# Kernel optimization log

Hardware: AMD Instinct MI355X
Metric: run time of the kernel (lower is better)

The kernel has to match this reference:

```python
import jax, jax.numpy as jnp
import numpy as np

N_NODES = 100000
N_EDGES = 1600000
D_IN, D_H1, D_H2 = 128, 64, 16


def setup_inputs() -> dict:
    key = jax.random.key(0)
    ks = jax.random.split(key, 12)
    def glorot(k, shape):
        fan_in, fan_out = shape
        lim = np.sqrt(6.0 / (fan_in + fan_out)).astype(np.float32)
        return jax.random.uniform(k, shape, jnp.float32, -lim, lim)
    x = jax.random.normal(ks[0], (N_NODES, D_IN), jnp.float32)
    edge_index = jax.random.randint(ks[1], (2, N_EDGES), 0, N_NODES, jnp.int64)
    return {
        "x": x,
        "edge_index": edge_index,
        # SAGEConv1: lin_l (neighbor agg, has bias), lin_r (root, no bias) -- stored (in,out)
        "w1_l": glorot(ks[2], (D_IN, D_H1)),
        "w1_r": glorot(ks[3], (D_IN, D_H1)),
        "b1": jnp.zeros((D_H1,), jnp.float32),
        # SAGEConv2
        "w2_l": glorot(ks[4], (D_H1, D_H2)),
        "w2_r": glorot(ks[5], (D_H1, D_H2)),
        "b2": jnp.zeros((D_H2,), jnp.float32),
        # MLP head
        "fc1_w": glorot(ks[6], (D_H2, 8)),
        "fc1_b": jnp.zeros((8,), jnp.float32),
        "fc2_w": glorot(ks[7], (8, 1)),
        "fc2_b": jnp.zeros((1,), jnp.float32),
    }


def _sage_conv(h, src, dst, n_nodes, w_l, w_r, b):
    # mean aggregation of source-node features into destination nodes
    msgs = h[src]                                                  # [E, d]
    agg = jax.ops.segment_sum(msgs, dst, num_segments=n_nodes)     # [N, d]
    deg = jax.ops.segment_sum(jnp.ones((src.shape[0],), h.dtype), dst,
                              num_segments=n_nodes)                # [N]
    mean = agg / jnp.maximum(deg, 1.0)[:, None]
    return mean @ w_l + h @ w_r + b


def reference(x, edge_index, w1_l, w1_r, b1, w2_l, w2_r, b2,
              fc1_w, fc1_b, fc2_w, fc2_b):
    src, dst = edge_index[0], edge_index[1]
    n = x.shape[0]
    h = _sage_conv(x, src, dst, n, w1_l, w1_r, b1)   # [N, 64]
    h = _sage_conv(h, src, dst, n, w2_l, w2_r, b2)   # [N, 16]
    # embedding_mlp on edge endpoint embeddings
    e = h[src] * h[dst]                              # [E, 16]
    out = (e @ fc1_w + fc1_b) @ fc2_w + fc2_b        # [E, 1]
    return jax.nn.sigmoid(out)
```

## Files before the change

kernel.cpp:

```cpp
#include <hip/hip_runtime.h>
#include <hip/hip_fp16.h>
#include <math.h>

#define NN 100000
#define NE 1600000

#define BSH  9
#define BKN  512
#define NB   196
#define ABLK 128
#define EPB  ((NE + ABLK - 1) / ABLK)
#define GEMMB ((NN + 63) / 64)
#define GBLK ((GEMMB + 1) / 2)
#define LDST 136

typedef __attribute__((ext_vector_type(8))) short bf16x8;
typedef __attribute__((ext_vector_type(4))) float f32x4;

__device__ __forceinline__ unsigned short f2bf(float f) {
    unsigned u = __builtin_bit_cast(unsigned, f);
    u += 0x7fffu + ((u >> 16) & 1u);
    return (unsigned short)(u >> 16);
}
__device__ __forceinline__ float bf2f(unsigned short h) {
    unsigned u = ((unsigned)h) << 16;
    return __builtin_bit_cast(float, u);
}
__device__ __forceinline__ float2 unpackh2(unsigned w) {
    const __half2 h = __builtin_bit_cast(__half2, w);
    return __half22float2(h);
}

__global__ __launch_bounds__(256) void fused0(const int* __restrict__ dst,
    const float* __restrict__ w1l, const float* __restrict__ w1r,
    const float* __restrict__ w2l, const float* __restrict__ w2r,
    const float* __restrict__ b1, const float* __restrict__ fc1w,
    const float* __restrict__ fc1b, const float* __restrict__ fc2w,
    const float* __restrict__ fc2b, int* __restrict__ mat,
    unsigned short* __restrict__ ATh, unsigned short* __restrict__ ATl,
    float* __restrict__ cbuf)
{
    __shared__ int h[NB];
    __shared__ float sl[64], sr[64];
    const int t = threadIdx.x;
    if (blockIdx.x < ABLK) {
        for (int i = t; i < NB; i += 256) h[i] = 0;
        __syncthreads();
        const int a = blockIdx.x;
        const int beg = a * EPB;
        const int end = (beg + EPB < NE) ? beg + EPB : NE;
        int e = beg + t;
        for (; e + 3 * 256 < end; e += 4 * 256) {
            const int d0 = dst[e], d1 = dst[e + 256], d2 = dst[e + 512], d3 = dst[e + 768];
            atomicAdd(&h[d0 >> BSH], 1);
            atomicAdd(&h[d1 >> BSH], 1);
            atomicAdd(&h[d2 >> BSH], 1);
            atomicAdd(&h[d3 >> BSH], 1);
        }
        for (; e < end; e += 256)
            atomicAdd(&h[dst[e] >> BSH], 1);
        __syncthreads();
        for (int i = t; i < NB; i += 256) mat[(size_t)i * ABLK + a] = h[i];
        return;
    }
    if (blockIdx.x < ABLK + 128) {
        const int k = blockIdx.x - ABLK;
        const int j = t;
        if (j < 64) { sl[j] = w1l[k * 64 + j]; sr[j] = w1r[k * 64 + j]; }
        __syncthreads();
        if (j < 64) {
            const int sel = j >> 4, jj = j & 15;
            const float* row = (sel < 2) ? sl : sr;
            const float* w2  = (sel & 1) ? w2r : w2l;
            float acc = 0.f;
#pragma unroll
            for (int m = 0; m < 64; ++m) acc = fmaf(row[m], w2[m * 16 + jj], acc);
            const unsigned short hh = f2bf(acc);
            ATh[j * 128 + k] = hh;
            ATl[j * 128 + k] = f2bf(acc - bf2f(hh));
        }
        return;
    }
    const int j = t;
    if (j < 16) {
        float a = 0.f;
        for (int m = 0; m < 64; ++m) a = fmaf(b1[m], w2l[m * 16 + j], a);
        cbuf[j] = a;
    } else if (j < 32) {
        const int jj = j - 16;
        float a = 0.f;
        for (int m = 0; m < 64; ++m) a = fmaf(b1[m], w2r[m * 16 + jj], a);
        cbuf[j] = a;
    } else if (j < 48) {
        const int k = j - 32;
        float a = 0.f;
        for (int m = 0; m < 8; ++m) a = fmaf(fc1w[k * 8 + m], fc2w[m], a);
        cbuf[j] = a;
    } else if (j == 48) {
        float a = fc2b[0];
        for (int m = 0; m < 8; ++m) a = fmaf(fc1b[m], fc2w[m], a);
        cbuf[48] = a;
    }
}

__global__ __launch_bounds__(256) void scan_all(int* __restrict__ mat,
    int* __restrict__ bbase)
{
    __shared__ int s[256];
    const int t = threadIdx.x;
    int run = 0;
    if (t < NB) {
        int* col = mat + (size_t)t * ABLK;
        for (int a = 0; a < ABLK; ++a) { const int v = col[a]; col[a] = run; run += v; }
    }
    s[t] = (t < NB) ? run : 0;
    __syncthreads();
    for (int off = 1; off < 256; off <<= 1) {
        const int u = (t >= off) ? s[t - off] : 0;
        __syncthreads();
        s[t] += u;
        __syncthreads();
    }
    if (t < NB) bbase[t] = s[t] - run;
    if (t == NB - 1) bbase[NB] = s[t];
}

__global__ __launch_bounds__(512) void fused1(const int* __restrict__ src,
    const int* __restrict__ dst, const int* __restrict__ mat,
    const int* __restrict__ bbase, unsigned* __restrict__ part,
    const float* __restrict__ x, const unsigned short* __restrict__ ATh,
    const unsigned short* __restrict__ ATl, signed char* __restrict__ p8,
    float* __restrict__ pscale, __half* __restrict__ qh)
{
    __shared__ unsigned short sAh[64 * LDST];
    __shared__ unsigned short sAl[64 * LDST];
    __shared__ int cur[NB];
    const int tid = threadIdx.x;

    if (blockIdx.x < ABLK) {
        const int a = blockIdx.x;
        for (int i = tid; i < NB; i += 512)
            cur[i] = mat[(size_t)i * ABLK + a] + bbase[i];
        __syncthreads();
        const int beg = a * EPB;
        const int end = (beg + EPB < NE) ? beg + EPB : NE;
        int e = beg + tid;
        for (; e + 3 * 512 < end; e += 4 * 512) {
            const int s0 = src[e],          d0 = dst[e];
            const int s1 = src[e + 512],    d1 = dst[e + 512];
            const int s2 = src[e + 1024],   d2 = dst[e + 1024];
            const int s3 = src[e + 1536],   d3 = dst[e + 1536];
            const int p0 = atomicAdd(&cur[d0 >> BSH], 1);
            const int p1 = atomicAdd(&cur[d1 >> BSH], 1);
            const int p2 = atomicAdd(&cur[d2 >> BSH], 1);
            const int p3 = atomicAdd(&cur[d3 >> BSH], 1);
            part[p0] = ((unsigned)s0 << BSH) | (unsigned)(d0 & (BKN - 1));
            part[p1] = ((unsigned)s1 << BSH) | (unsigned)(d1 & (BKN - 1));
            part[p2] = ((unsigned)s2 << BSH) | (unsigned)(d2 & (BKN - 1));
            part[p3] = ((unsigned)s3 << BSH) | (unsigned)(d3 & (BKN - 1));
        }
        for (; e < end; e += 512) {
            const int s = src[e], d = dst[e];
            const int pos = atomicAdd(&cur[d >> BSH], 1);
            part[pos] = ((unsigned)s << BSH) | (unsigned)(d & (BKN - 1));
        }
        return;
    }

    for (int i = tid; i < 1024; i += 512) {
        const int row = i >> 4, ch = i & 15;
        const uint4 vh = *(const uint4*)(ATh + row * 128 + ch * 8);
        const uint4 vl = *(const uint4*)(ATl + row * 128 + ch * 8);
        *(uint4*)(sAh + row * LDST + ch * 8) = vh;
        *(uint4*)(sAl + row * LDST + ch * 8) = vl;
    }
    __syncthreads();

    const int wave8 = tid >> 6;
    const int tile = (blockIdx.x - ABLK) * 2 + (wave8 >> 2);
    const int wave = wave8 & 3;
    const int lane = tid & 63;
    const int lr = lane & 15;
    const int lg = lane >> 4;

    bf16x8 bh[4][4], bl[4][4];
#pragma unroll
    for (int ct = 0; ct < 4; ++ct) {
        const int col = ct * 16 + lr;
#pragma unroll
        for (int ks = 0; ks < 4; ++ks) {
            const int k0 = ks * 32 + lg * 8;
            bh[ct][ks] = *(const bf16x8*)(sAh + col * LDST + k0);
            bl[ct][ks] = *(const bf16x8*)(sAl + col * LDST + k0);
        }
    }

    if (tile >= GEMMB) return;
    const int tilebase = tile * 64;
    const int xrowidx = tilebase + wave * 16 + lr;
    const float* xrow = x + (size_t)(xrowidx < NN ? xrowidx : NN - 1) * 128;

    f32x4 acc[4] = {f32x4{0,0,0,0}, f32x4{0,0,0,0}, f32x4{0,0,0,0}, f32x4{0,0,0,0}};
#pragma unroll
    for (int ks = 0; ks < 4; ++ks) {
        const int k0 = ks * 32 + lg * 8;
        const float4 v0 = *(const float4*)(xrow + k0);
        const float4 v1 = *(const float4*)(xrow + k0 + 4);
        const float vv[8] = {v0.x, v0.y, v0.z, v0.w, v1.x, v1.y, v1.z, v1.w};
        bf16x8 xh, xl;
#pragma unroll
        for (int j = 0; j < 8; ++j) {
            const unsigned short h = f2bf(vv[j]);
            xh[j] = (short)h;
            xl[j] = (short)f2bf(vv[j] - bf2f(h));
        }
#pragma unroll
        for (int ct = 0; ct < 4; ++ct) {
            acc[ct] = __builtin_amdgcn_mfma_f32_16x16x32_bf16(xh, bh[ct][ks], acc[ct], 0, 0, 0);
            acc[ct] = __builtin_amdgcn_mfma_f32_16x16x32_bf16(xh, bl[ct][ks], acc[ct], 0, 0, 0);
            acc[ct] = __builtin_amdgcn_mfma_f32_16x16x32_bf16(xl, bh[ct][ks], acc[ct], 0, 0, 0);
        }
    }

#pragma unroll
    for (int rg = 0; rg < 4; ++rg) {
        float m = fmaxf(fabsf(acc[0][rg]), fabsf(acc[1][rg]));
#pragma unroll
        for (int d = 1; d < 16; d <<= 1) m = fmaxf(m, __shfl_xor(m, d, 64));
        m = fmaxf(m, 1e-20f);
        const float scl = m * (1.0f / 127.0f);
        const float inv = 127.0f / m;
        const int nrow = tilebase + wave * 16 + lg * 4 + rg;
        if (nrow < NN) {
            const int q0 = __float2int_rn(acc[0][rg] * inv);
            const int q1 = __float2int_rn(acc[1][rg] * inv);
            p8[(size_t)nrow * 32 + lr]      = (signed char)q0;
            p8[(size_t)nrow * 32 + 16 + lr] = (signed char)q1;
            if (lr == 0) pscale[nrow] = scl;
            qh[(size_t)nrow * 32 + lr]      = __float2half(acc[2][rg]);
            qh[(size_t)nrow * 32 + 16 + lr] = __float2half(acc[3][rg]);
        }
    }
}

__global__ __launch_bounds__(512) void partB_build(const unsigned* __restrict__ part,
    const int* __restrict__ bbase, int* __restrict__ rowptr, int* __restrict__ cols)
{
    __shared__ int h[BKN];
    __shared__ int cur[BKN];
    __shared__ int wsum[8];
    const int b = blockIdx.x;
    const int t = threadIdx.x;
    const int beg = bbase[b], end = bbase[b + 1];
    h[t] = 0;
    __syncthreads();
    {
        int e = beg + t;
        for (; e + 3 * 512 < end; e += 4 * 512) {
            const unsigned w0 = part[e], w1 = part[e + 512];
            const unsigned w2 = part[e + 1024], w3 = part[e + 1536];
            atomicAdd(&h[w0 & (BKN - 1u)], 1);
            atomicAdd(&h[w1 & (BKN - 1u)], 1);
            atomicAdd(&h[w2 & (BKN - 1u)], 1);
            atomicAdd(&h[w3 & (BKN - 1u)], 1);
        }
        for (; e < end; e += 512)
            atomicAdd(&h[part[e] & (BKN - 1u)], 1);
    }
    __syncthreads();
    const int v = h[t];
    int inc = v;
#pragma unroll
    for (int d = 1; d < 64; d <<= 1) {
        const int u = __shfl_up(inc, d, 64);
        if ((t & 63) >= d) inc += u;
    }
    if ((t & 63) == 63) wsum[t >> 6] = inc;
    __syncthreads();
    int woff = 0;
    for (int w = 0; w < (t >> 6); ++w) woff += wsum[w];
    const int excl = inc + woff - v;
    cur[t] = excl;
    const int node = b * BKN + t;
    if (node < NN) rowptr[node] = beg + excl;
    if (b == NB - 1 && t == 0) rowptr[NN] = NE;
    __syncthreads();
    {
        int e = beg + t;
        for (; e + 3 * 512 < end; e += 4 * 512) {
            const unsigned w0 = part[e], w1 = part[e + 512];
            const unsigned w2 = part[e + 1024], w3 = part[e + 1536];
            const int p0 = atomicAdd(&cur[w0 & (BKN - 1u)], 1);
            const int p1 = atomicAdd(&cur[w1 & (BKN - 1u)], 1);
            const int p2 = atomicAdd(&cur[w2 & (BKN - 1u)], 1);
            const int p3 = atomicAdd(&cur[w3 & (BKN - 1u)], 1);
            cols[beg + p0] = (int)(w0 >> BSH);
            cols[beg + p1] = (int)(w1 >> BSH);
            cols[beg + p2] = (int)(w2 >> BSH);
            cols[beg + p3] = (int)(w3 >> BSH);
        }
        for (; e < end; e += 512) {
            const unsigned w = part[e];
            const int pos = atomicAdd(&cur[w & (BKN - 1u)], 1);
            cols[beg + pos] = (int)(w >> BSH);
        }
    }
}

__global__ __launch_bounds__(256) void agg1_csr(const int* __restrict__ rowptr,
    const int* __restrict__ cols, const signed char* __restrict__ p8,
    const float* __restrict__ pscale, const __half* __restrict__ qh,
    const float* __restrict__ cbuf, __half* __restrict__ g, __half* __restrict__ r)
{
    const int node = blockIdx.x * 8 + (threadIdx.x >> 5);
    if (node >= NN) return;
    const int lane = threadIdx.x & 31;
    const int es = lane >> 2;
    const int k  = lane & 3;
    const int beg = rowptr[node], end = rowptr[node + 1];
    const int deg = end - beg;
    const int grpbase = threadIdx.x & 32;
    const int myc = (lane < deg) ? cols[beg + lane] : 0;
    const uint2* p64 = (const uint2*)p8;
    float a0 = 0.f, a1 = 0.f, a2 = 0.f, a3 = 0.f;
    float a4 = 0.f, a5 = 0.f, a6 = 0.f, a7 = 0.f;
#pragma unroll 2
    for (int base = 0; base < deg; base += 8) {
        const int idx = base + es;
        const bool valid = idx < deg;
        int s;
        if (idx < 32) s = __shfl(myc, grpbase + idx, 64);
        else          s = cols[beg + (valid ? idx : deg - 1)];
        const float scl = valid ? pscale[s] : 0.f;
        const uint2 w = p64[(size_t)s * 4 + k];
        a0 = fmaf((float)(signed char)(w.x & 0xffu), scl, a0);
        a1 = fmaf((float)(signed char)((w.x >> 8) & 0xffu), scl, a1);
        a2 = fmaf((float)(signed char)((w.x >> 16) & 0xffu), scl, a2);
        a3 = fmaf((float)(signed char)(w.x >> 24), scl, a3);
        a4 = fmaf((float)(signed char)(w.y & 0xffu), scl, a4);
        a5 = fmaf((float)(signed char)((w.y >> 8) & 0xffu), scl, a5);
        a6 = fmaf((float)(signed char)((w.y >> 16) & 0xffu), scl, a6);
        a7 = fmaf((float)(signed char)(w.y >> 24), scl, a7);
    }
#pragma unroll
    for (int d = 4; d <= 16; d <<= 1) {
        a0 += __shfl_xor(a0, d, 64); a1 += __shfl_xor(a1, d, 64);
        a2 += __shfl_xor(a2, d, 64); a3 += __shfl_xor(a3, d, 64);
        a4 += __shfl_xor(a4, d, 64); a5 += __shfl_xor(a5, d, 64);
        a6 += __shfl_xor(a6, d, 64); a7 += __shfl_xor(a7, d, 64);
    }
    if (es == 0) {
        const float dg = (float)deg;
        const float inv = 1.0f / fmaxf(dg, 1.0f);
        const uint4 qw = *(const uint4*)(qh + (size_t)node * 32 + 8 * k);
        const float2 q0 = unpackh2(qw.x), q1 = unpackh2(qw.y);
        const float2 q2 = unpackh2(qw.z), q3 = unpackh2(qw.w);
        const float4 cb0 = *(const float4*)(cbuf + 8 * k);
        const float4 cb1 = *(const float4*)(cbuf + 8 * k + 4);
        const float v0 = fmaf(a0, inv, q0.x + cb0.x);
        const float v1 = fmaf(a1, inv, q0.y + cb0.y);
        const float v2 = fmaf(a2, inv, q1.x + cb0.z);
        const float v3 = fmaf(a3, inv, q1.y + cb0.w);
        const float v4 = fmaf(a4, inv, q2.x + cb1.x);
        const float v5 = fmaf(a5, inv, q2.y + cb1.y);
        const float v6 = fmaf(a6, inv, q3.x + cb1.z);
        const float v7 = fmaf(a7, inv, q3.y + cb1.w);
        uint4 ow;
        ow.x = __builtin_bit_cast(unsigned, __floats2half2_rn(v0, v1));
        ow.y = __builtin_bit_cast(unsigned, __floats2half2_rn(v2, v3));
        ow.z = __builtin_bit_cast(unsigned, __floats2half2_rn(v4, v5));
        ow.w = __builtin_bit_cast(unsigned, __floats2half2_rn(v6, v7));
        if (k < 2) *(uint4*)(g + (size_t)node * 16 + 8 * k) = ow;
        else       *(uint4*)(r + (size_t)node * 16 + 8 * (k - 2)) = ow;
    }
}

__global__ __launch_bounds__(256) void agg2_csr(const int* __restrict__ rowptr,
    const int* __restrict__ cols, const __half* __restrict__ g,
    const __half* __restrict__ r, const float* __restrict__ b2,
    __half* __restrict__ h2)
{
    const int node = blockIdx.x * 8 + (threadIdx.x >> 5);
    if (node >= NN) return;
    const int lane = threadIdx.x & 31;
    const int es = lane >> 2;
    const int k  = lane & 3;
    const int beg = rowptr[node], end = rowptr[node + 1];
    const int deg = end - beg;
    const int grpbase = threadIdx.x & 32;
    const int myc = (lane < deg) ? cols[beg + lane] : 0;
    const uint2* g64 = (const uint2*)g;
    float a0 = 0.f, a1 = 0.f, a2 = 0.f, a3 = 0.f;
#pragma unroll 2
    for (int base = 0; base < deg; base += 8) {
        const int idx = base + es;
        const bool valid = idx < deg;
        int s;
        if (idx < 32) s = __shfl(myc, grpbase + idx, 64);
        else          s = cols[beg + (valid ? idx : deg - 1)];
        const float m = valid ? 1.0f : 0.0f;
        const uint2 w = g64[(size_t)s * 4 + k];
        const float2 v0 = unpackh2(w.x);
        const float2 v1 = unpackh2(w.y);
        a0 = fmaf(v0.x, m, a0);
        a1 = fmaf(v0.y, m, a1);
        a2 = fmaf(v1.x, m, a2);
        a3 = fmaf(v1.y, m, a3);
    }
#pragma unroll
    for (int d = 4; d <= 16; d <<= 1) {
        a0 += __shfl_xor(a0, d, 64); a1 += __shfl_xor(a1, d, 64);
        a2 += __shfl_xor(a2, d, 64); a3 += __shfl_xor(a3, d, 64);
    }
    if (es == 0) {
        const float dg = (float)deg;
        const float inv = 1.0f / fmaxf(dg, 1.0f);
        const uint2 rw = ((const uint2*)r)[(size_t)node * 4 + k];
        const float2 r0 = unpackh2(rw.x), r1 = unpackh2(rw.y);
        const float4 bb = *(const float4*)(b2 + 4 * k);
        const float v0 = fmaf(a0, inv, r0.x + bb.x);
        const float v1 = fmaf(a1, inv, r0.y + bb.y);
        const float v2 = fmaf(a2, inv, r1.x + bb.z);
        const float v3 = fmaf(a3, inv, r1.y + bb.w);
        uint2 ow;
        ow.x = __builtin_bit_cast(unsigned, __floats2half2_rn(v0, v1));
        ow.y = __builtin_bit_cast(unsigned, __floats2half2_rn(v2, v3));
        ((uint2*)h2)[(size_t)node * 4 + k] = ow;
    }
}

__global__ __launch_bounds__(256) void edge_mlp(const int* __restrict__ src,
    const int* __restrict__ dst, const __half* __restrict__ h2,
    const float* __restrict__ cbuf, float* __restrict__ out)
{
    __shared__ float sv[17];
    if (threadIdx.x < 16) sv[threadIdx.x] = cbuf[32 + threadIdx.x];
    if (threadIdx.x == 16) sv[16] = cbuf[48];
    __syncthreads();
    const int ebase = blockIdx.x * 1024 + threadIdx.x;
#pragma unroll
    for (int u = 0; u < 4; ++u) {
        const int e = ebase + u * 256;
        if (e >= NE) return;
        const int s = src[e], d = dst[e];
        const uint4* hs = (const uint4*)(h2 + (size_t)s * 16);
        const uint4* hd = (const uint4*)(h2 + (size_t)d * 16);
        const uint4 a0 = hs[0], a1 = hs[1];
        const uint4 b0 = hd[0], b1 = hd[1];
        const unsigned aw[8] = {a0.x, a0.y, a0.z, a0.w, a1.x, a1.y, a1.z, a1.w};
        const unsigned bw[8] = {b0.x, b0.y, b0.z, b0.w, b1.x, b1.y, b1.z, b1.w};
        float acc = sv[16];
#pragma unroll
        for (int qq = 0; qq < 8; ++qq) {
            const float2 a = unpackh2(aw[qq]);
            const float2 b = unpackh2(bw[qq]);
            acc = fmaf(a.x * b.x, sv[qq * 2 + 0], acc);
            acc = fmaf(a.y * b.y, sv[qq * 2 + 1], acc);
        }
        out[e] = 1.0f / (1.0f + __expf(-acc));
    }
}

extern "C" void kernel_launch(void* const* d_in, const int* in_sizes, int n_in,
                              void* d_out, int out_size, void* d_ws, size_t ws_size,
                              hipStream_t stream)
{
    const float* x    = (const float*)d_in[0];
    const int*   ei   = (const int*)d_in[1];
    const float* w1l  = (const float*)d_in[2];
    const float* w1r  = (const float*)d_in[3];
    const float* b1   = (const float*)d_in[4];
    const float* w2l  = (const float*)d_in[5];
    const float* w2r  = (const float*)d_in[6];
    const float* b2   = (const float*)d_in[7];
    const float* fc1w = (const float*)d_in[8];
    const float* fc1b = (const float*)d_in[9];
    const float* fc2w = (const float*)d_in[10];
    const float* fc2b = (const float*)d_in[11];
    float* out = (float*)d_out;

    const int* src = ei;
    const int* dst = ei + NE;

    int* W = (int*)d_ws;
    size_t o = 0;
#define ALIGN16() o = (o + 15) & ~(size_t)15
    int* mat    = W + o; o += (size_t)NB * ABLK; ALIGN16();
    int* bbase  = W + o; o += NB + 1;            ALIGN16();
    int* rowptr = W + o; o += NN + 1;            ALIGN16();
    unsigned* part = (unsigned*)(W + o); o += NE; ALIGN16();
    int* cols   = W + o; o += NE;                ALIGN16();
    unsigned short* ATh = (unsigned short*)(W + o); o += 4096; ALIGN16();
    unsigned short* ATl = (unsigned short*)(W + o); o += 4096; ALIGN16();
    float* cbuf = (float*)(W + o); o += 64;      ALIGN16();
    signed char* p8 = (signed char*)(W + o); o += (size_t)NN * 8;  ALIGN16();
    float* pscale   = (float*)(W + o); o += NN;  ALIGN16();
    __half* qh  = (__half*)(W + o); o += (size_t)NN * 16; ALIGN16();
    __half* g   = (__half*)(W + o); o += (size_t)NN * 8;  ALIGN16();
    __half* r   = (__half*)(W + o); o += (size_t)NN * 8;  ALIGN16();
    __half* h2  = (__half*)(W + o); o += (size_t)NN * 8;  ALIGN16();

    fused0<<<ABLK + 129, 256, 0, stream>>>(dst, w1l, w1r, w2l, w2r, b1,
                                           fc1w, fc1b, fc2w, fc2b, mat, ATh, ATl, cbuf);
    scan_all<<<1, 256, 0, stream>>>(mat, bbase);
    fused1<<<ABLK + GBLK, 512, 0, stream>>>(src, dst, mat, bbase, part,
                                            x, ATh, ATl, p8, pscale, qh);
    partB_build<<<NB, 512, 0, stream>>>(part, bbase, rowptr, cols);
    agg1_csr<<<(NN + 7) / 8, 256, 0, stream>>>(rowptr, cols, p8, pscale, qh, cbuf, g, r);
    agg2_csr<<<(NN + 7) / 8, 256, 0, stream>>>(rowptr, cols, g, r, b2, h2);
    edge_mlp<<<(NE + 1023) / 1024, 256, 0, stream>>>(src, dst, h2, cbuf, out);
}
```

Baseline: 126.2 us.

## Fold bucket scan into partition kernel and halve destination bucket width

Removes the single-block scan_all launch. Each partition block of fused1 now recomputes its own column prefix and a block-wide scan of bucket totals, and block 0 writes bbase. The bucket size drops from 512 to 256 nodes, giving 391 buckets, so partB_build runs more, smaller blocks with half its threads idle. This trades one kernel launch plus a serial scan for redundant per-block scan work in every partition block.

After: 122.1 us. 3.2% less time.

```diff
diff --git a/kernel.cpp b/kernel.cpp
--- a/kernel.cpp
+++ b/kernel.cpp
@@ -5,9 +5,9 @@
 #define NN 100000
 #define NE 1600000
 
-#define BSH  9
-#define BKN  512
-#define NB   196
+#define BSH  8
+#define BKN  256
+#define NB   391
 #define ABLK 128
 #define EPB  ((NE + ABLK - 1) / ABLK)
 #define GEMMB ((NN + 63) / 64)
@@ -103,31 +103,9 @@
     }
 }
 
-__global__ __launch_bounds__(256) void scan_all(int* __restrict__ mat,
-    int* __restrict__ bbase)
-{
-    __shared__ int s[256];
-    const int t = threadIdx.x;
-    int run = 0;
-    if (t < NB) {
-        int* col = mat + (size_t)t * ABLK;
-        for (int a = 0; a < ABLK; ++a) { const int v = col[a]; col[a] = run; run += v; }
-    }
-    s[t] = (t < NB) ? run : 0;
-    __syncthreads();
-    for (int off = 1; off < 256; off <<= 1) {
-        const int u = (t >= off) ? s[t - off] : 0;
-        __syncthreads();
-        s[t] += u;
-        __syncthreads();
-    }
-    if (t < NB) bbase[t] = s[t] - run;
-    if (t == NB - 1) bbase[NB] = s[t];
-}
-
 __global__ __launch_bounds__(512) void fused1(const int* __restrict__ src,
     const int* __restrict__ dst, const int* __restrict__ mat,
-    const int* __restrict__ bbase, unsigned* __restrict__ part,
+    int* __restrict__ bbase, unsigned* __restrict__ part,
     const float* __restrict__ x, const unsigned short* __restrict__ ATh,
     const unsigned short* __restrict__ ATl, signed char* __restrict__ p8,
     float* __restrict__ pscale, __half* __restrict__ qh)
@@ -135,13 +113,41 @@
     __shared__ unsigned short sAh[64 * LDST];
     __shared__ unsigned short sAl[64 * LDST];
     __shared__ int cur[NB];
+    __shared__ int tot[NB];
+    __shared__ int sarr[512];
     const int tid = threadIdx.x;
 
     if (blockIdx.x < ABLK) {
         const int a = blockIdx.x;
-        for (int i = tid; i < NB; i += 512)
-            cur[i] = mat[(size_t)i * ABLK + a] + bbase[i];
+        for (int i = tid; i < NB; i += 512) {
+            const int* col = mat + (size_t)i * ABLK;
+            int run = 0, mypre = 0;
+            for (int a2 = 0; a2 < ABLK; ++a2) {
+                const int v = col[a2];
+                mypre += (a2 < a) ? v : 0;
+                run += v;
+            }
+            tot[i] = run;
+            cur[i] = mypre;
+        }
         __syncthreads();
+        const int myrun = (tid < NB) ? tot[tid] : 0;
+        sarr[tid] = myrun;
+        __syncthreads();
+        for (int off = 1; off < 512; off <<= 1) {
+            const int u = (tid >= off) ? sarr[tid - off] : 0;
+            __syncthreads();
+            sarr[tid] += u;
+            __syncthreads();
+        }
+        if (tid < NB) {
+            const int base = sarr[tid] - myrun;
+            cur[tid] += base;
+            if (a == 0) bbase[tid] = base;
+        }
+        if (a == 0 && tid == NB - 1) bbase[NB] = sarr[tid];
+        __syncthreads();
+
         const int beg = a * EPB;
         const int end = (beg + EPB < NE) ? beg + EPB : NE;
         int e = beg + tid;
@@ -252,7 +258,7 @@
     const int b = blockIdx.x;
     const int t = threadIdx.x;
     const int beg = bbase[b], end = bbase[b + 1];
-    h[t] = 0;
+    if (t < BKN) h[t] = 0;
     __syncthreads();
     {
         int e = beg + t;
@@ -268,7 +274,7 @@
             atomicAdd(&h[part[e] & (BKN - 1u)], 1);
     }
     __syncthreads();
-    const int v = h[t];
+    const int v = (t < BKN) ? h[t] : 0;
     int inc = v;
 #pragma unroll
     for (int d = 1; d < 64; d <<= 1) {
@@ -280,9 +286,11 @@
     int woff = 0;
     for (int w = 0; w < (t >> 6); ++w) woff += wsum[w];
     const int excl = inc + woff - v;
-    cur[t] = excl;
-    const int node = b * BKN + t;
-    if (node < NN) rowptr[node] = beg + excl;
+    if (t < BKN) {
+        cur[t] = excl;
+        const int node = b * BKN + t;
+        if (node < NN) rowptr[node] = beg + excl;
+    }
     if (b == NB - 1 && t == 0) rowptr[NN] = NE;
     __syncthreads();
     {
@@ -502,7 +510,6 @@
 
     fused0<<<ABLK + 129, 256, 0, stream>>>(dst, w1l, w1r, w2l, w2r, b1,
                                            fc1w, fc1b, fc2w, fc2b, mat, ATh, ATl, cbuf);
-    scan_all<<<1, 256, 0, stream>>>(mat, bbase);
     fused1<<<ABLK + GBLK, 512, 0, stream>>>(src, dst, mat, bbase, part,
                                             x, ATh, ATl, p8, pscale, qh);
     partB_build<<<NB, 512, 0, stream>>>(part, bbase, rowptr, cols);
```
